# Optimization experiments

Hardware: AMD Instinct MI355X
Metric: run time of the kernel (lower is better)

The kernel has to match this reference:

```python
import jax, jax.numpy as jnp
import numpy as np

N_NODES = 50000
N_EDGES = 600000
D_IN = 128
D_OUT = 128
K_HOPS = 2  # Gra_inc(2)


def _gcn_norm(edge_index, edge_weight, num_nodes, dtype):
    # Add self-loops (weight 1.0) and compute symmetric GCN normalization.
    loop = jnp.arange(num_nodes, dtype=edge_index.dtype)
    row = jnp.concatenate([edge_index[0], loop])  # source
    col = jnp.concatenate([edge_index[1], loop])  # destination
    w = jnp.concatenate([edge_weight, jnp.ones((num_nodes,), dtype=dtype)])
    deg = jax.ops.segment_sum(w, col, num_segments=num_nodes)
    dinv = jnp.where(deg > 0, jax.lax.rsqrt(deg), jnp.zeros_like(deg))
    norm = dinv[row] * w * dinv[col]  # [E + N]
    return row, col, norm


def setup_inputs() -> dict:
    key = jax.random.key(0)
    k1, k2, k3, k4 = jax.random.split(key, 4)
    x = jax.random.normal(k1, (N_NODES, D_IN), dtype=jnp.float32)
    edge_index = jax.random.randint(k2, (2, N_EDGES), 0, N_NODES, dtype=jnp.int64)
    edge_weight = jax.random.uniform(k3, (N_EDGES,), dtype=jnp.float32)
    # Linear(in,out,bias=False) weight, PyTorch layout [out, in]
    W = jax.random.normal(k4, (D_OUT, D_IN), dtype=jnp.float32) * (1.0 / np.sqrt(D_IN))
    return {"x": x, "edge_index": edge_index, "edge_weight": edge_weight, "W": W}


def reference(x, edge_index, edge_weight, W):
    num_nodes = x.shape[0]
    h = x @ W.T  # lin11: [N, D_OUT]
    row, col, norm = _gcn_norm(edge_index, edge_weight, num_nodes, h.dtype)
    # Gra_inc(2): K=2 hops of normalized sparse propagation h <- A_hat @ h
    for _ in range(K_HOPS):
        msgs = norm[:, None] * h[row]  # gather + scale, [E+N, D_OUT]
        h = jax.ops.segment_sum(msgs, col, num_segments=num_nodes)
    return h  # bias is None (bias=False)
```

## Files before the change

kernel.cpp:

```cpp
#include <hip/hip_runtime.h>

typedef unsigned long long u64;
typedef unsigned int u32;
typedef _Float16 f16;

#define NN 50000
#define NE 600000
#define D  128
#define NWAVE 3125
#define GGEMM 782
#define EPB 2048
#define NB_P 293
#define NP 196
#define NSTRIP 2
#define GS 1563

typedef __attribute__((ext_vector_type(8))) __bf16 bf16x8;
typedef __attribute__((ext_vector_type(8))) unsigned short us8;
typedef __attribute__((ext_vector_type(8))) f16 f16x8;
typedef __attribute__((ext_vector_type(4))) float f32x4;

__device__ __forceinline__ unsigned short f2bf(float f) {
    u32 u = __float_as_uint(f);
    return (unsigned short)((u + 0x7FFFu + ((u >> 16) & 1u)) >> 16);
}
__device__ __forceinline__ float bf2f(unsigned short h) {
    return __uint_as_float((u32)h << 16);
}

__global__ __launch_bounds__(256) void wprep(const float* __restrict__ W,
                                             us8* __restrict__ Whi,
                                             us8* __restrict__ Wlo) {
    const int i = blockIdx.x * 256 + threadIdx.x;
    if (i < 2048) {
        const int lane = i & 63, nt = (i >> 6) & 7, kc4 = i >> 9;
        const float* p =
            W + (size_t)(nt * 16 + (lane & 15)) * D + kc4 * 32 + (lane >> 4) * 8;
        float v[8];
        *(float4*)&v[0] = *(const float4*)p;
        *(float4*)&v[4] = *(const float4*)(p + 4);
        us8 hi, lo;
#pragma unroll
        for (int j = 0; j < 8; ++j) {
            const unsigned short hb = f2bf(v[j]);
            hi[j] = hb;
            lo[j] = f2bf(v[j] - bf2f(hb));
        }
        Whi[i] = hi;
        Wlo[i] = lo;
    }
}

__global__ __launch_bounds__(256) void gemm_count(
    const float* __restrict__ x, const us8* __restrict__ Whi,
    const us8* __restrict__ Wlo, f16* __restrict__ h16,
    const int* __restrict__ col, int* __restrict__ cnt) {
    const int t = threadIdx.x;
    __shared__ us8 WH[2048];

    if (blockIdx.x < NB_P) {
        int* bins = (int*)WH;
        for (int i = t; i < NP; i += 256) bins[i] = 0;
        __syncthreads();
        const int e0 = blockIdx.x * EPB + t;
#pragma unroll
        for (int s = 0; s < 8; ++s) {
            const int e = e0 + s * 256;
            if (e < NE) atomicAdd(&bins[col[e] >> 8], 1);
        }
        __syncthreads();
        for (int i = t; i < NP; i += 256)
            cnt[i * NB_P + blockIdx.x] = bins[i];
        return;
    }

    const int g = (blockIdx.x - NB_P) * 4 + (t >> 6);
    const int lane = t & 63;
    const int gc = (g < NWAVE) ? g : (NWAVE - 1);
    const int row0 = gc * 16;

    const float* px = x + (size_t)(row0 + (lane & 15)) * D + (lane >> 4) * 8;
    float4 ar[8];
#pragma unroll
    for (int c = 0; c < 4; ++c) {
        ar[2 * c]     = *(const float4*)(px + c * 32);
        ar[2 * c + 1] = *(const float4*)(px + c * 32 + 4);
    }

#pragma unroll
    for (int i = 0; i < 8; ++i) WH[t + i * 256] = Whi[t + i * 256];
    __syncthreads();
    if (g >= NWAVE) return;

    f32x4 acc[8];
#pragma unroll
    for (int nt = 0; nt < 8; ++nt) acc[nt] = (f32x4){0.f, 0.f, 0.f, 0.f};

#pragma unroll
    for (int c = 0; c < 4; ++c) {
        bf16x8 blv[8];
#pragma unroll
        for (int nt = 0; nt < 8; ++nt)
            blv[nt] = *(const bf16x8*)&Wlo[c * 512 + nt * 64 + lane];

        float v[8];
        *(float4*)&v[0] = ar[2 * c];
        *(float4*)&v[4] = ar[2 * c + 1];
        us8 hiu, lou;
#pragma unroll
        for (int j = 0; j < 8; ++j) {
            const unsigned short hb = f2bf(v[j]);
            hiu[j] = hb;
            lou[j] = f2bf(v[j] - bf2f(hb));
        }
        const bf16x8 ah = *(const bf16x8*)&hiu;
        const bf16x8 al = *(const bf16x8*)&lou;
#pragma unroll
        for (int nt = 0; nt < 8; ++nt) {
            const bf16x8 bh = *(const bf16x8*)&WH[c * 512 + nt * 64 + lane];
            acc[nt] = __builtin_amdgcn_mfma_f32_16x16x32_bf16(ah, bh, acc[nt], 0, 0, 0);
            acc[nt] = __builtin_amdgcn_mfma_f32_16x16x32_bf16(al, bh, acc[nt], 0, 0, 0);
            acc[nt] = __builtin_amdgcn_mfma_f32_16x16x32_bf16(ah, blv[nt], acc[nt], 0, 0, 0);
        }
    }

    const int q = lane >> 4, cl = lane & 15;
#pragma unroll
    for (int nt = 0; nt < 8; ++nt) {
        f16* o = h16 + (size_t)(nt >> 2) * ((size_t)NN * 64) + (nt & 3) * 16 + cl;
#pragma unroll
        for (int r = 0; r < 4; ++r)
            o[(size_t)(row0 + q * 4 + r) * 64] = (f16)acc[nt][r];
    }
}

__global__ __launch_bounds__(256) void scan_blocks(int* __restrict__ cnt,
                                                   int* __restrict__ totals) {
    __shared__ int sw[256];
    const int p = blockIdx.x, tid = threadIdx.x;
    const int i0 = 2 * tid, i1 = 2 * tid + 1;
    const int a0 = (i0 < NB_P) ? cnt[p * NB_P + i0] : 0;
    const int a1 = (i1 < NB_P) ? cnt[p * NB_P + i1] : 0;
    const int pair = a0 + a1;
    sw[tid] = pair;
    __syncthreads();
    for (int off = 1; off < 256; off <<= 1) {
        int tv = (tid >= off) ? sw[tid - off] : 0;
        __syncthreads();
        if (tid >= off) sw[tid] += tv;
        __syncthreads();
    }
    const int excl = sw[tid] - pair;
    if (i0 < NB_P) cnt[p * NB_P + i0] = excl;
    if (i1 < NB_P) cnt[p * NB_P + i1] = excl + a0;
    if (tid == 255) totals[p] = sw[255];
}

__global__ __launch_bounds__(256) void scan_parts(const int* __restrict__ totals,
                                                  int* __restrict__ binbase,
                                                  int* __restrict__ base) {
    __shared__ int sw[256];
    const int tid = threadIdx.x;
    const int v = (tid < NP) ? totals[tid] : 0;
    sw[tid] = v;
    __syncthreads();
    for (int off = 1; off < 256; off <<= 1) {
        int tv = (tid >= off) ? sw[tid - off] : 0;
        __syncthreads();
        if (tid >= off) sw[tid] += tv;
        __syncthreads();
    }
    if (tid < NP) binbase[tid] = sw[tid] - v;
    if (tid == NP - 1) {
        binbase[NP] = sw[tid];
        base[NN] = sw[tid];
    }
}

__global__ __launch_bounds__(256) void scatter_k(
    const int* __restrict__ row, const int* __restrict__ col,
    const float* __restrict__ w, const int* __restrict__ cnt,
    const int* __restrict__ binbase, u64* __restrict__ part) {
    __shared__ int bins[NP];
    __shared__ int off0[NP];
    const int b = blockIdx.x, t = threadIdx.x;
    for (int i = t; i < NP; i += 256) {
        bins[i] = 0;
        off0[i] = binbase[i] + cnt[i * NB_P + b];
    }
    __syncthreads();
    const int e0 = b * EPB + t;
#pragma unroll
    for (int s = 0; s < 8; ++s) {
        const int e = e0 + s * 256;
        if (e < NE) {
            const int c = col[e];
            const int p = c >> 8;
            const int lr = atomicAdd(&bins[p], 1);
            part[off0[p] + lr] = ((u64)__float_as_uint(w[e]) << 32) |
                                 ((u32)row[e] << 8) | (u32)(c & 255);
        }
    }
}

__global__ __launch_bounds__(256) void csr_k(
    const u64* __restrict__ part, const int* __restrict__ binbase,
    int* __restrict__ base, float* __restrict__ dinv,
    int2* __restrict__ sedge) {
    __shared__ u32 cntL[256];
    __shared__ float wsL[256];
    __shared__ int curL[256];
    __shared__ int sw[256];
    const int p = blockIdx.x, tid = threadIdx.x;
    const int eb = binbase[p], ee = binbase[p + 1];

    cntL[tid] = 0u;
    wsL[tid] = 0.f;
    __syncthreads();
    for (int e = eb + tid; e < ee; e += 256) {
        const u64 pk = part[e];
        const int cl = (int)(pk & 255u);
        atomicAdd(&cntL[cl], 1u);
        atomicAdd(&wsL[cl], __uint_as_float((u32)(pk >> 32)));
    }
    __syncthreads();

    const int node = p * 256 + tid;
    const float di = rsqrtf(1.0f + wsL[tid]);
    const int myc = (int)cntL[tid];
    sw[tid] = myc;
    __syncthreads();
    for (int off = 1; off < 256; off <<= 1) {
        int tv = (tid >= off) ? sw[tid - off] : 0;
        __syncthreads();
        if (tid >= off) sw[tid] += tv;
        __syncthreads();
    }
    const int excl = sw[tid] - myc;
    if (node < NN) {
        dinv[node] = di;
        base[node] = eb + excl;
    }
    __syncthreads();
    wsL[tid] = di;
    curL[tid] = excl;
    __syncthreads();

    for (int e = eb + tid; e < ee; e += 256) {
        const u64 pk = part[e];
        const int cl = (int)(pk & 255u);
        const int r = (int)((pk >> 8) & 0xFFFFu);
        const float wv = __uint_as_float((u32)(pk >> 32));
        const int lr = atomicAdd(&curL[cl], 1);
        int2 ed;
        ed.x = r;
        ed.y = __float_as_int(wv * wsL[cl]);
        sedge[eb + lr] = ed;
    }
}

__global__ __launch_bounds__(256) void norm_k(int2* __restrict__ sedge,
                                              const float* __restrict__ dinv) {
    const int e = blockIdx.x * 256 + threadIdx.x;
    if (e < NE) {
        const int2 ed = sedge[e];
        sedge[e].y = __float_as_int(__int_as_float(ed.y) * dinv[ed.x]);
    }
}

template <int OUTF>
__global__ __launch_bounds__(256) void hop_kernel(
    const f16* __restrict__ src, f16* __restrict__ dst16,
    float* __restrict__ dstf, const int2* __restrict__ sedge,
    const int* __restrict__ base, const float* __restrict__ dinv) {
    const int node = blockIdx.x * 32 + (threadIdx.x >> 3);
    if (node >= NN) return;
    const int strip = blockIdx.y;
    const int lo8 = (threadIdx.x & 7) * 8;
    const f16* hs = src + (size_t)strip * ((size_t)NN * 64) + lo8;

    const int b = base[node];
    const int k = base[node + 1] - b;

    float acc[8] = {0.f, 0.f, 0.f, 0.f, 0.f, 0.f, 0.f, 0.f};
#pragma unroll 4
    for (int j = 0; j < k; ++j) {
        const int2 ed = sedge[b + j];
        const f16x8 hv = *(const f16x8*)(hs + (size_t)ed.x * 64);
        const float nm = __int_as_float(ed.y);
#pragma unroll
        for (int i = 0; i < 8; ++i) acc[i] = fmaf(nm, (float)hv[i], acc[i]);
    }
    const float di = dinv[node];
    const float d2 = di * di;
    const f16x8 sv = *(const f16x8*)(hs + (size_t)node * 64);
#pragma unroll
    for (int i = 0; i < 8; ++i) acc[i] = fmaf(d2, (float)sv[i], acc[i]);

    if (OUTF) {
        float* o = dstf + (size_t)node * D + strip * 64 + lo8;
        *(float4*)&o[0] = make_float4(acc[0], acc[1], acc[2], acc[3]);
        *(float4*)&o[4] = make_float4(acc[4], acc[5], acc[6], acc[7]);
    } else {
        f16x8 ov;
#pragma unroll
        for (int i = 0; i < 8; ++i) ov[i] = (f16)acc[i];
        *(f16x8*)(dst16 + (size_t)strip * ((size_t)NN * 64) + (size_t)node * 64 + lo8) = ov;
    }
}

extern "C" void kernel_launch(void* const* d_in, const int* in_sizes, int n_in,
                              void* d_out, int out_size, void* d_ws,
                              size_t ws_size, hipStream_t stream) {
    const float* x  = (const float*)d_in[0];
    const int*   ei = (const int*)d_in[1];
    const float* w  = (const float*)d_in[2];
    const float* W  = (const float*)d_in[3];
    float* out = (float*)d_out;

    const int* row = ei;
    const int* col = ei + NE;

    f16* h16a = (f16*)d_ws;
    f16* h16b = h16a + (size_t)2 * NN * 64;
    u64* part = (u64*)h16b;
    us8* Whi = (us8*)(h16b + (size_t)2 * NN * 64);
    us8* Wlo = Whi + 2048;
    int* cnt = (int*)(Wlo + 2048);
    int* totals = cnt + NP * NB_P;
    int* binbase = totals + NP;
    int* base = binbase + NP + 1;
    float* dinv = (float*)(base + NN + 1);
    int2* sedge = (int2*)(dinv + NN);

    const int gE = (NE + 255) / 256;

    hipMemsetAsync(cnt, 0, (size_t)NP * NB_P * sizeof(int), stream);
    wprep<<<8, 256, 0, stream>>>(W, Whi, Wlo);
    gemm_count<<<NB_P + GGEMM, 256, 0, stream>>>(x, Whi, Wlo, h16a, col, cnt);
    scan_blocks<<<NP, 256, 0, stream>>>(cnt, totals);
    scan_parts<<<1, 256, 0, stream>>>(totals, binbase, base);
    scatter_k<<<NB_P, 256, 0, stream>>>(row, col, w, cnt, binbase, part);
    csr_k<<<NP, 256, 0, stream>>>(part, binbase, base, dinv, sedge);
    norm_k<<<gE, 256, 0, stream>>>(sedge, dinv);

    hop_kernel<0><<<dim3(GS, NSTRIP), 256, 0, stream>>>(h16a, h16b, nullptr,
                                                        sedge, base, dinv);
    hop_kernel<1><<<dim3(GS, NSTRIP), 256, 0, stream>>>(h16b, nullptr, out,
                                                        sedge, base, dinv);
}
```

Measured before the change: 107.8 us.

## Fuse W prep into GEMM, merge scans via ticket, fold norm into hops

Removes the wprep kernel, so each GEMM block converts W to bf16 hi/lo splits directly into shared memory. The two scan kernels are merged into one using an atomic ticket, with the last block doing the partition scan. The norm_k pass and the memset are dropped, and the source-side dinv multiply moves into the hop gather loops. This cuts launch count and a full pass over the edges, but every GEMM block now repeats the W conversion and each hop does an extra dinv gather per edge.

```diff
diff --git a/kernel.cpp b/kernel.cpp
--- a/kernel.cpp
+++ b/kernel.cpp
@@ -28,14 +28,50 @@
     return __uint_as_float((u32)h << 16);
 }
 
-__global__ __launch_bounds__(256) void wprep(const float* __restrict__ W,
-                                             us8* __restrict__ Whi,
-                                             us8* __restrict__ Wlo) {
-    const int i = blockIdx.x * 256 + threadIdx.x;
-    if (i < 2048) {
-        const int lane = i & 63, nt = (i >> 6) & 7, kc4 = i >> 9;
+__global__ __launch_bounds__(256) void gemm_count(
+    const float* __restrict__ x, const float* __restrict__ W,
+    f16* __restrict__ h16, const int* __restrict__ col,
+    int* __restrict__ cnt, u32* __restrict__ done) {
+    const int t = threadIdx.x;
+    __shared__ us8 WH[2048];
+    __shared__ us8 WL[2048];
+
+    if (blockIdx.x < NB_P) {
+        if (blockIdx.x == 0 && t == 0) *done = 0u;
+        int* bins = (int*)WH;
+        for (int i = t; i < NP; i += 256) bins[i] = 0;
+        __syncthreads();
+        const int e0 = blockIdx.x * EPB + t;
+#pragma unroll
+        for (int s = 0; s < 8; ++s) {
+            const int e = e0 + s * 256;
+            if (e < NE) atomicAdd(&bins[col[e] >> 8], 1);
+        }
+        __syncthreads();
+        for (int i = t; i < NP; i += 256)
+            cnt[i * NB_P + blockIdx.x] = bins[i];
+        return;
+    }
+
+    const int g = (blockIdx.x - NB_P) * 4 + (t >> 6);
+    const int lane = t & 63;
+    const int gc = (g < NWAVE) ? g : (NWAVE - 1);
+    const int row0 = gc * 16;
+
+    const float* px = x + (size_t)(row0 + (lane & 15)) * D + (lane >> 4) * 8;
+    float4 ar[8];
+#pragma unroll
+    for (int c = 0; c < 4; ++c) {
+        ar[2 * c]     = *(const float4*)(px + c * 32);
+        ar[2 * c + 1] = *(const float4*)(px + c * 32 + 4);
+    }
+
+#pragma unroll
+    for (int s = 0; s < 8; ++s) {
+        const int i = s * 256 + t;
+        const int ln = i & 63, nt = (i >> 6) & 7, kc4 = i >> 9;
         const float* p =
-            W + (size_t)(nt * 16 + (lane & 15)) * D + kc4 * 32 + (lane >> 4) * 8;
+            W + (size_t)(nt * 16 + (ln & 15)) * D + kc4 * 32 + (ln >> 4) * 8;
         float v[8];
         *(float4*)&v[0] = *(const float4*)p;
         *(float4*)&v[4] = *(const float4*)(p + 4);
@@ -46,63 +82,18 @@
             hi[j] = hb;
             lo[j] = f2bf(v[j] - bf2f(hb));
         }
-        Whi[i] = hi;
-        Wlo[i] = lo;
-    }
-}
-
-__global__ __launch_bounds__(256) void gemm_count(
-    const float* __restrict__ x, const us8* __restrict__ Whi,
-    const us8* __restrict__ Wlo, f16* __restrict__ h16,
-    const int* __restrict__ col, int* __restrict__ cnt) {
-    const int t = threadIdx.x;
-    __shared__ us8 WH[2048];
-
-    if (blockIdx.x < NB_P) {
-        int* bins = (int*)WH;
-        for (int i = t; i < NP; i += 256) bins[i] = 0;
-        __syncthreads();
-        const int e0 = blockIdx.x * EPB + t;
-#pragma unroll
-        for (int s = 0; s < 8; ++s) {
-            const int e = e0 + s * 256;
-            if (e < NE) atomicAdd(&bins[col[e] >> 8], 1);
-        }
-        __syncthreads();
-        for (int i = t; i < NP; i += 256)
-            cnt[i * NB_P + blockIdx.x] = bins[i];
-        return;
-    }
-
-    const int g = (blockIdx.x - NB_P) * 4 + (t >> 6);
-    const int lane = t & 63;
-    const int gc = (g < NWAVE) ? g : (NWAVE - 1);
-    const int row0 = gc * 16;
-
-    const float* px = x + (size_t)(row0 + (lane & 15)) * D + (lane >> 4) * 8;
-    float4 ar[8];
+        WH[i] = hi;
+        WL[i] = lo;
+    }
+    __syncthreads();
+    if (g >= NWAVE) return;
+
+    f32x4 acc[8];
+#pragma unroll
+    for (int nt = 0; nt < 8; ++nt) acc[nt] = (f32x4){0.f, 0.f, 0.f, 0.f};
+
 #pragma unroll
     for (int c = 0; c < 4; ++c) {
-        ar[2 * c]     = *(const float4*)(px + c * 32);
-        ar[2 * c + 1] = *(const float4*)(px + c * 32 + 4);
-    }
-
-#pragma unroll
-    for (int i = 0; i < 8; ++i) WH[t + i * 256] = Whi[t + i * 256];
-    __syncthreads();
-    if (g >= NWAVE) return;
-
-    f32x4 acc[8];
-#pragma unroll
-    for (int nt = 0; nt < 8; ++nt) acc[nt] = (f32x4){0.f, 0.f, 0.f, 0.f};
-
-#pragma unroll
-    for (int c = 0; c < 4; ++c) {
-        bf16x8 blv[8];
-#pragma unroll
-        for (int nt = 0; nt < 8; ++nt)
-            blv[nt] = *(const bf16x8*)&Wlo[c * 512 + nt * 64 + lane];
-
         float v[8];
         *(float4*)&v[0] = ar[2 * c];
         *(float4*)&v[4] = ar[2 * c + 1];
@@ -118,9 +109,10 @@
 #pragma unroll
         for (int nt = 0; nt < 8; ++nt) {
             const bf16x8 bh = *(const bf16x8*)&WH[c * 512 + nt * 64 + lane];
+            const bf16x8 bl = *(const bf16x8*)&WL[c * 512 + nt * 64 + lane];
             acc[nt] = __builtin_amdgcn_mfma_f32_16x16x32_bf16(ah, bh, acc[nt], 0, 0, 0);
             acc[nt] = __builtin_amdgcn_mfma_f32_16x16x32_bf16(al, bh, acc[nt], 0, 0, 0);
-            acc[nt] = __builtin_amdgcn_mfma_f32_16x16x32_bf16(ah, blv[nt], acc[nt], 0, 0, 0);
+            acc[nt] = __builtin_amdgcn_mfma_f32_16x16x32_bf16(ah, bl, acc[nt], 0, 0, 0);
         }
     }
 
@@ -134,9 +126,12 @@
     }
 }
 
-__global__ __launch_bounds__(256) void scan_blocks(int* __restrict__ cnt,
-                                                   int* __restrict__ totals) {
+__global__ __launch_bounds__(256) void scan_fused(
+    int* __restrict__ cnt, int* __restrict__ totals,
+    int* __restrict__ binbase, int* __restrict__ base,
+    u32* __restrict__ done) {
     __shared__ int sw[256];
+    __shared__ u32 ticket;
     const int p = blockIdx.x, tid = threadIdx.x;
     const int i0 = 2 * tid, i1 = 2 * tid + 1;
     const int a0 = (i0 < NB_P) ? cnt[p * NB_P + i0] : 0;
@@ -153,15 +148,15 @@
     const int excl = sw[tid] - pair;
     if (i0 < NB_P) cnt[p * NB_P + i0] = excl;
     if (i1 < NB_P) cnt[p * NB_P + i1] = excl + a0;
-    if (tid == 255) totals[p] = sw[255];
-}
-
-__global__ __launch_bounds__(256) void scan_parts(const int* __restrict__ totals,
-                                                  int* __restrict__ binbase,
-                                                  int* __restrict__ base) {
-    __shared__ int sw[256];
-    const int tid = threadIdx.x;
-    const int v = (tid < NP) ? totals[tid] : 0;
+    if (tid == 0) {
+        atomicExch(&totals[p], sw[255]);
+        __threadfence();
+        ticket = atomicAdd(done, 1u);
+    }
+    __syncthreads();
+    if (ticket != NP - 1) return;
+
+    const int v = (tid < NP) ? atomicAdd(&totals[tid], 0) : 0;
     sw[tid] = v;
     __syncthreads();
     for (int off = 1; off < 256; off <<= 1) {
@@ -259,15 +254,6 @@
     }
 }
 
-__global__ __launch_bounds__(256) void norm_k(int2* __restrict__ sedge,
-                                              const float* __restrict__ dinv) {
-    const int e = blockIdx.x * 256 + threadIdx.x;
-    if (e < NE) {
-        const int2 ed = sedge[e];
-        sedge[e].y = __float_as_int(__int_as_float(ed.y) * dinv[ed.x]);
-    }
-}
-
 template <int OUTF>
 __global__ __launch_bounds__(256) void hop_kernel(
     const f16* __restrict__ src, f16* __restrict__ dst16,
@@ -287,7 +273,7 @@
     for (int j = 0; j < k; ++j) {
         const int2 ed = sedge[b + j];
         const f16x8 hv = *(const f16x8*)(hs + (size_t)ed.x * 64);
-        const float nm = __int_as_float(ed.y);
+        const float nm = __int_as_float(ed.y) * dinv[ed.x];
 #pragma unroll
         for (int i = 0; i < 8; ++i) acc[i] = fmaf(nm, (float)hv[i], acc[i]);
     }
@@ -324,25 +310,18 @@
     f16* h16a = (f16*)d_ws;
     f16* h16b = h16a + (size_t)2 * NN * 64;
     u64* part = (u64*)h16b;
-    us8* Whi = (us8*)(h16b + (size_t)2 * NN * 64);
-    us8* Wlo = Whi + 2048;
-    int* cnt = (int*)(Wlo + 2048);
+    int* cnt = (int*)(h16b + (size_t)2 * NN * 64);
     int* totals = cnt + NP * NB_P;
-    int* binbase = totals + NP;
+    u32* done = (u32*)(totals + NP);
+    int* binbase = (int*)(done + 1);
     int* base = binbase + NP + 1;
     float* dinv = (float*)(base + NN + 1);
     int2* sedge = (int2*)(dinv + NN);
 
-    const int gE = (NE + 255) / 256;
-
-    hipMemsetAsync(cnt, 0, (size_t)NP * NB_P * sizeof(int), stream);
-    wprep<<<8, 256, 0, stream>>>(W, Whi, Wlo);
-    gemm_count<<<NB_P + GGEMM, 256, 0, stream>>>(x, Whi, Wlo, h16a, col, cnt);
-    scan_blocks<<<NP, 256, 0, stream>>>(cnt, totals);
-    scan_parts<<<1, 256, 0, stream>>>(totals, binbase, base);
+    gemm_count<<<NB_P + GGEMM, 256, 0, stream>>>(x, W, h16a, col, cnt, done);
+    scan_fused<<<NP, 256, 0, stream>>>(cnt, totals, binbase, base, done);
     scatter_k<<<NB_P, 256, 0, stream>>>(row, col, w, cnt, binbase, part);
     csr_k<<<NP, 256, 0, stream>>>(part, binbase, base, dinv, sedge);
-    norm_k<<<gE, 256, 0, stream>>>(sedge, dinv);
 
     hop_kernel<0><<<dim3(GS, NSTRIP), 256, 0, stream>>>(h16a, h16b, nullptr,
                                                         sedge, base, dinv);
```

New measurement: 106.2 us. No clear change (-1.5%).
